# Kernel tuning notes

Hardware: AMD Instinct MI355X
Metric: run time of the kernel (lower is better)

Reference implementation:

```python
import jax, jax.numpy as jnp
import numpy as np

V, S, D, H = 32000, 1024, 768, 3072
EPS = 1e-5


def pos_encoding(seq_len, dim, dtype=jnp.float32):
    # pe[pos, i] = sin(pos/10000^(i/dim)) if i even else cos(pos/10000^(i/dim))
    pos = jnp.arange(seq_len, dtype=dtype)[:, None]
    i = jnp.arange(dim, dtype=dtype)[None, :]
    ang = pos / jnp.power(jnp.asarray(10000.0, dtype), i / dim)
    even = (jnp.arange(dim) % 2 == 0)[None, :]
    return jnp.where(even, jnp.sin(ang), jnp.cos(ang))


def layernorm2d(x, w, b):
    # normalizes over last two dims (token_size, input_dim), affine params [S, D]
    m = jnp.mean(x, axis=(-2, -1), keepdims=True)
    v = jnp.mean((x - m) ** 2, axis=(-2, -1), keepdims=True)
    return (x - m) / jnp.sqrt(v + EPS) * w + b


def setup_inputs() -> dict:
    key = jax.random.key(0)
    ks = jax.random.split(key, 16)
    sc = 0.02
    emb = jax.random.normal(ks[0], (V, D), jnp.float32) * sc
    emb = emb.at[0].set(0.0)  # padding_idx=0
    inp = {
        "x": jax.random.randint(ks[1], (8, S), 0, V),
        "emb": emb,
        "Wq": jax.random.normal(ks[2], (D, H), jnp.float32) * sc,
        "bq": jnp.zeros((H,), jnp.float32),
        "Wk": jax.random.normal(ks[3], (D, H), jnp.float32) * sc,
        "bk": jnp.zeros((H,), jnp.float32),
        "Wv": jax.random.normal(ks[4], (D, H), jnp.float32) * sc,
        "bv": jnp.zeros((H,), jnp.float32),
        "Wo": jax.random.normal(ks[5], (H, D), jnp.float32) * sc,
        "bo": jnp.zeros((D,), jnp.float32),
        "W1": jax.random.normal(ks[6], (D, H), jnp.float32) * sc,
        "b1": jnp.zeros((H,), jnp.float32),
        "W2": jax.random.normal(ks[7], (H, D), jnp.float32) * sc,
        "b2": jnp.zeros((D,), jnp.float32),
        "ln1_w": jnp.ones((S, D), jnp.float32),
        "ln1_b": jnp.zeros((S, D), jnp.float32),
        "ln2_w": jnp.ones((S, D), jnp.float32),
        "ln2_b": jnp.zeros((S, D), jnp.float32),
    }
    return inp


def reference(x, emb, Wq, bq, Wk, bk, Wv, bv, Wo, bo, W1, b1, W2, b2, ln1_w, ln1_b, ln2_w, ln2_b):
    y = emb[x]                                   # [B, S, D]
    y = y + pos_encoding(y.shape[1], y.shape[2], y.dtype)
    # unscaled self-attention (no 1/sqrt(d) factor, faithful to source)
    q = y @ Wq + bq
    k = y @ Wk + bk
    v = y @ Wv + bv
    attn = jax.nn.softmax(jnp.einsum("bsh,bth->bst", q, k), axis=-1)
    a = jnp.einsum("bst,bth->bsh", attn, v) @ Wo + bo
    y = layernorm2d(y + a, ln1_w, ln1_b)
    # FFN: GELU applied AFTER second linear (faithful to source)
    f = jax.nn.gelu((y @ W1 + b1) @ W2 + b2, approximate=False)
    y = layernorm2d(y + f, ln2_w, ln2_b)
    return y
```

## Files before the change

kernel.cpp:

```cpp
#include <hip/hip_runtime.h>
#include <hip/hip_fp16.h>

#define DI __device__ __forceinline__

typedef _Float16 f16x8 __attribute__((ext_vector_type(8)));
typedef float f32x4 __attribute__((ext_vector_type(4)));

struct alignas(8) h4 { __half x, y, z, w; };

DI void async16(const void* g, void* l) {
  __builtin_amdgcn_global_load_lds(
      (__attribute__((address_space(1))) void*)g,
      (__attribute__((address_space(3))) void*)l, 16, 0, 0);
}

DI float waveReduceSum(float v) {
#pragma unroll
  for (int i = 1; i < 64; i <<= 1) v += __shfl_xor(v, i);
  return v;
}
DI float waveReduceMax(float v) {
#pragma unroll
  for (int i = 1; i < 64; i <<= 1) v = fmaxf(v, __shfl_xor(v, i));
  return v;
}

DI float gelu_exact(float x) { return 0.5f * x * (1.f + erff(x * 0.70710678118654752f)); }

template <typename CT, bool BIAS, bool BROW>
__global__ __launch_bounds__(512, 2) void gemm_nt8(
    const __half* __restrict__ A, int lda, long long sA,
    const __half* __restrict__ Bt, int ldb, long long sB,
    const float* __restrict__ bias, long long sBias,
    CT* __restrict__ C, int ldc, long long sC,
    int nT, int K) {
  __shared__ __align__(16) __half As[2][16384];
  __shared__ __align__(16) __half Bs[2][16384];

  const int tid = threadIdx.x;
  const int wave = tid >> 6, lane = tid & 63;

  const int gsz = 4 * nT;
  const int g = blockIdx.x / gsz, r = blockIdx.x % gsz;
  const int m0 = (g * 4 + (r & 3)) * 256;
  const int n0 = (r >> 2) * 256;

  A += (long long)blockIdx.z * sA;
  Bt += (long long)blockIdx.z * sB;
  C += (long long)blockIdx.z * sC;
  if constexpr (BIAS || BROW) bias += (long long)blockIdx.z * sBias;

  const int wm = wave >> 2, wn = wave & 3;

  f32x4 acc[8][4];
#pragma unroll
  for (int i = 0; i < 8; ++i)
#pragma unroll
    for (int j = 0; j < 4; ++j) acc[i][j] = (f32x4){0.f, 0.f, 0.f, 0.f};

  const int srow = tid >> 3;
  const int gc = (tid & 7) ^ (srow & 7);
  const __half* Ag = A + (size_t)(m0 + srow) * lda + gc * 8;
  const __half* Bg = Bt + (size_t)(n0 + srow) * ldb + gc * 8;
  const size_t a64 = (size_t)64 * lda, b64 = (size_t)64 * ldb;
  char* AsW = (char*)As + wave * 1024;
  char* BsW = (char*)Bs + wave * 1024;

#define STG_A(t)                                                      \
  {                                                                   \
    const __half* s_ = Ag + (t) * 64;                                 \
    char* d_ = AsW + (((t) & 1) ? 32768 : 0);                         \
    async16(s_, d_);                                                  \
    async16(s_ + a64, d_ + 8192);                                     \
    async16(s_ + 2 * a64, d_ + 16384);                                \
    async16(s_ + 3 * a64, d_ + 24576);                                \
  }
#define STG_B(t)                                                      \
  {                                                                   \
    const __half* s_ = Bg + (t) * 64;                                 \
    char* d_ = BsW + (((t) & 1) ? 32768 : 0);                         \
    async16(s_, d_);                                                  \
    async16(s_ + b64, d_ + 8192);                                     \
    async16(s_ + 2 * b64, d_ + 16384);                                \
    async16(s_ + 3 * b64, d_ + 24576);                                \
  }

  const int ml = lane & 15, q = lane >> 4, lx = lane & 7;
  const int co0 = (q ^ lx) * 16, co1 = co0 ^ 64;
  const char* Ar = (const char*)As + wm * 16384 + ml * 128;
  const char* Br = (const char*)Bs + (wn >> 1) * 16384 + (wn & 1) * 8192 + ml * 128;

  const int nt = K >> 6;
  STG_A(0);
  STG_B(0);
  if (nt > 1) {
    STG_A(1);
    STG_B(1);
    asm volatile("s_waitcnt vmcnt(8)" ::: "memory");
  } else {
    asm volatile("s_waitcnt vmcnt(0)" ::: "memory");
  }
  __builtin_amdgcn_s_barrier();

  for (int t = 0; t < nt; ++t) {
    const int pb = (t & 1) ? 32768 : 0;
    const char* Ap = Ar + pb;
    const char* Bp = Br + pb;
    f16x8 a0[4], a1[4], a2[4], a3[4], b0[4], b1[4];

#pragma unroll
    for (int i = 0; i < 4; ++i) a0[i] = *(const f16x8*)(Ap + i * 2048 + co0);
#pragma unroll
    for (int j = 0; j < 4; ++j) b0[j] = *(const f16x8*)(Bp + j * 2048 + co0);
    __builtin_amdgcn_s_barrier();
    asm volatile("s_waitcnt lgkmcnt(0)" ::: "memory");
    __builtin_amdgcn_s_setprio(1);
#pragma unroll
    for (int i = 0; i < 4; ++i)
#pragma unroll
      for (int j = 0; j < 4; ++j)
        acc[i][j] = __builtin_amdgcn_mfma_f32_16x16x32_f16(a0[i], b0[j], acc[i][j], 0, 0, 0);
    __builtin_amdgcn_s_setprio(0);
    __builtin_amdgcn_s_barrier();

#pragma unroll
    for (int i = 0; i < 4; ++i) a1[i] = *(const f16x8*)(Ap + (4 + i) * 2048 + co0);
#pragma unroll
    for (int j = 0; j < 4; ++j) b1[j] = *(const f16x8*)(Bp + j * 2048 + co1);
    __builtin_amdgcn_s_barrier();
    asm volatile("s_waitcnt lgkmcnt(0)" ::: "memory");
    __builtin_amdgcn_s_setprio(1);
#pragma unroll
    for (int i = 0; i < 4; ++i)
#pragma unroll
      for (int j = 0; j < 4; ++j)
        acc[4 + i][j] = __builtin_amdgcn_mfma_f32_16x16x32_f16(a1[i], b0[j], acc[4 + i][j], 0, 0, 0);
    __builtin_amdgcn_s_setprio(0);
    __builtin_amdgcn_s_barrier();

#pragma unroll
    for (int i = 0; i < 4; ++i) a2[i] = *(const f16x8*)(Ap + i * 2048 + co1);
#pragma unroll
    for (int i = 0; i < 4; ++i) a3[i] = *(const f16x8*)(Ap + (4 + i) * 2048 + co1);
    if (t + 2 < nt) STG_B(t + 2);
    __builtin_amdgcn_s_barrier();
    asm volatile("s_waitcnt lgkmcnt(0)" ::: "memory");
    __builtin_amdgcn_s_setprio(1);
#pragma unroll
    for (int i = 0; i < 4; ++i)
#pragma unroll
      for (int j = 0; j < 4; ++j)
        acc[i][j] = __builtin_amdgcn_mfma_f32_16x16x32_f16(a2[i], b1[j], acc[i][j], 0, 0, 0);
    __builtin_amdgcn_s_setprio(0);
    __builtin_amdgcn_s_barrier();

    if (t + 2 < nt) {
      STG_A(t + 2);
      asm volatile("s_waitcnt vmcnt(8)" ::: "memory");
    } else if (t + 1 < nt) {
      asm volatile("s_waitcnt vmcnt(0)" ::: "memory");
    }
    __builtin_amdgcn_s_barrier();
    __builtin_amdgcn_s_setprio(1);
#pragma unroll
    for (int i = 0; i < 4; ++i)
#pragma unroll
      for (int j = 0; j < 4; ++j)
        acc[4 + i][j] = __builtin_amdgcn_mfma_f32_16x16x32_f16(a3[i], b1[j], acc[4 + i][j], 0, 0, 0);
    __builtin_amdgcn_s_setprio(0);
    __builtin_amdgcn_s_barrier();
  }
#undef STG_A
#undef STG_B

#pragma unroll
  for (int j = 0; j < 4; ++j) {
    const int col = n0 + wn * 64 + j * 16 + ml;
    const float bcol = BIAS ? bias[col] : 0.f;
#pragma unroll
    for (int i = 0; i < 8; ++i) {
      const int row = m0 + wm * 128 + i * 16 + q * 4;
#pragma unroll
      for (int rr = 0; rr < 4; ++rr) {
        float v = acc[i][j][rr] + bcol;
        if constexpr (BROW) v += bias[row + rr];
        if constexpr (sizeof(CT) == 4)
          C[(size_t)(row + rr) * ldc + col] = v;
        else
          C[(size_t)(row + rr) * ldc + col] = __float2half(v);
      }
    }
  }
}

template <typename CT, bool BIAS, bool BROW>
__global__ __launch_bounds__(256) void gemm_nt(
    const __half* __restrict__ A, int lda, long long sA,
    const __half* __restrict__ Bt, int ldb, long long sB,
    const float* __restrict__ bias, long long sBias,
    CT* __restrict__ C, int ldc, long long sC,
    int nT, int K) {
  __shared__ __align__(16) __half As[128 * 64];
  __shared__ __align__(16) __half Bs[128 * 64];

  const int tid = threadIdx.x;
  const int wave = tid >> 6, lane = tid & 63;

  const int gsz = 8 * nT;
  const int g = blockIdx.x / gsz, r = blockIdx.x % gsz;
  const int m0 = (g * 8 + (r & 7)) * 128;
  const int n0 = (r >> 3) * 128;

  A += (long long)blockIdx.z * sA;
  Bt += (long long)blockIdx.z * sB;
  C += (long long)blockIdx.z * sC;
  if constexpr (BIAS || BROW) bias += (long long)blockIdx.z * sBias;
  const int wm = wave & 1, wn = wave >> 1;

  f32x4 acc[4][4];
#pragma unroll
  for (int i = 0; i < 4; ++i)
#pragma unroll
    for (int jj = 0; jj < 4; ++jj) acc[i][jj] = (f32x4){0.f, 0.f, 0.f, 0.f};

  const int srow = tid >> 3;
  const int gc = (tid & 7) ^ (srow & 7);
  const __half* Ag = A + (size_t)(m0 + srow) * lda + gc * 8;
  const __half* Bg = Bt + (size_t)(n0 + srow) * ldb + gc * 8;
  const size_t a32 = (size_t)32 * lda, b32 = (size_t)32 * ldb;
  char* AsW = (char*)As + wave * 1024;
  char* BsW = (char*)Bs + wave * 1024;

  const int ml = lane & 15, q = lane >> 4, lx = lane & 7;
  const int aoff = ((wm * 64 + ml) * 8 + (q ^ lx)) * 16;
  const int boff = ((wn * 64 + ml) * 8 + (q ^ lx)) * 16;

  for (int k0 = 0; k0 < K; k0 += 64) {
#pragma unroll
    for (int i = 0; i < 4; ++i) {
      async16(Ag + i * a32 + k0, AsW + i * 4096);
      async16(Bg + i * b32 + k0, BsW + i * 4096);
    }
    __syncthreads();
#pragma unroll
    for (int jj = 0; jj < 2; ++jj) {
      const char* Ab = (const char*)As + (jj ? (aoff ^ 64) : aoff);
      const char* Bb = (const char*)Bs + (jj ? (boff ^ 64) : boff);
      f16x8 af[4], bf[4];
#pragma unroll
      for (int i = 0; i < 4; ++i) {
        af[i] = *(const f16x8*)(Ab + i * 2048);
        bf[i] = *(const f16x8*)(Bb + i * 2048);
      }
#pragma unroll
      for (int i = 0; i < 4; ++i)
#pragma unroll
        for (int jn = 0; jn < 4; ++jn)
          acc[i][jn] = __builtin_amdgcn_mfma_f32_16x16x32_f16(af[i], bf[jn], acc[i][jn], 0, 0, 0);
    }
    __syncthreads();
  }

#pragma unroll
  for (int jj = 0; jj < 4; ++jj) {
    const int col = n0 + wn * 64 + jj * 16 + ml;
    const float bcol = BIAS ? bias[col] : 0.f;
#pragma unroll
    for (int i = 0; i < 4; ++i) {
      const int row = m0 + wm * 64 + i * 16 + q * 4;
#pragma unroll
      for (int rr = 0; rr < 4; ++rr) {
        float v = acc[i][jj][rr] + bcol;
        if constexpr (BROW) v += bias[row + rr];
        if constexpr (sizeof(CT) == 4)
          C[(size_t)(row + rr) * ldc + col] = v;
        else
          C[(size_t)(row + rr) * ldc + col] = __float2half(v);
      }
    }
  }
}

__global__ __launch_bounds__(256) void prep(
    const float* __restrict__ Wq, const float* __restrict__ Wk,
    const float* __restrict__ Wv, const float* __restrict__ W1,
    const float* __restrict__ Wo, const float* __restrict__ W2,
    const float* __restrict__ bq, const float* __restrict__ bk,
    __half* __restrict__ wD, __half* __restrict__ wB, __half* __restrict__ wC,
    __half* __restrict__ wA, float* __restrict__ bqk) {
  if (blockIdx.x == 2304) {
    if (blockIdx.y == 0)
      for (int i = threadIdx.x; i < 3072; i += 256) {
        bqk[i] = bq[i];
        bqk[3072 + i] = bk[i];
      }
    return;
  }
  __shared__ float t[32][33];
  const int tx = threadIdx.x & 31, ty = threadIdx.x >> 5;
  if (blockIdx.y < 4) {
    const float* in;
    __half* out;
    switch (blockIdx.y) {
      case 0: in = Wq; out = wD; break;
      case 1: in = Wk; out = wD + 3072 * 768; break;
      case 2: in = Wv; out = wB; break;
      default: in = W1; out = wC; break;
    }
    const int cb = blockIdx.x % 96, rb = blockIdx.x / 96;
    const int c = cb * 32 + tx, r0 = rb * 32;
#pragma unroll
    for (int i = 0; i < 32; i += 8) t[ty + i][tx] = in[(size_t)(r0 + ty + i) * 3072 + c];
    __syncthreads();
    const int oc = r0 + tx, o0 = cb * 32;
#pragma unroll
    for (int i = 0; i < 32; i += 8)
      out[(size_t)(o0 + ty + i) * 768 + oc] = __float2half(t[tx][ty + i]);
  } else {
    const float* in = (blockIdx.y == 5) ? W2 : Wo;
    __half* out = wA + ((blockIdx.y == 5) ? 3072 * 768 : 0);
    const int cb = blockIdx.x % 24, rb = blockIdx.x / 24;
    const int c = cb * 32 + tx, r0 = rb * 32;
#pragma unroll
    for (int i = 0; i < 32; i += 8) t[ty + i][tx] = in[(size_t)(r0 + ty + i) * 768 + c];
    __syncthreads();
    const int oc = r0 + tx, o0 = cb * 32;
#pragma unroll
    for (int i = 0; i < 32; i += 8)
      out[(size_t)(o0 + ty + i) * 3072 + oc] = __float2half(t[tx][ty + i]);
  }
}

__global__ __launch_bounds__(256) void embed_pos_kernel(
    const int* __restrict__ x, const float* __restrict__ emb,
    float* __restrict__ y, __half* __restrict__ yh) {
  const int row = blockIdx.x;
  const int s = row & 1023;
  const int tok = x[row];
  const float* ep = emb + (size_t)tok * 768;
  float* yp = y + (size_t)row * 768;
  __half* hp = yh + (size_t)row * 768;
  const float c = -13.287712379549449f / 768.f;
  for (int d = threadIdx.x; d < 768; d += 256) {
    float ang = (float)s * exp2f((float)d * c);
    float pe = (d & 1) ? cosf(ang) : sinf(ang);
    float v = ep[d] + pe;
    yp[d] = v;
    hp[d] = __float2half(v);
  }
}

__global__ __launch_bounds__(256) void softmax_rows(
    const float* __restrict__ L, __half* __restrict__ P) {
  const size_t row = blockIdx.x;
  const float4 x = ((const float4*)(L + row * 1024))[threadIdx.x];
  const int wave = threadIdx.x >> 6, lane = threadIdx.x & 63;
  float m = fmaxf(fmaxf(x.x, x.y), fmaxf(x.z, x.w));
  m = waveReduceMax(m);
  __shared__ float sm[4];
  __shared__ float ssum[4];
  if (lane == 0) sm[wave] = m;
  __syncthreads();
  m = fmaxf(fmaxf(sm[0], sm[1]), fmaxf(sm[2], sm[3]));
  float e0 = expf(x.x - m), e1 = expf(x.y - m), e2 = expf(x.z - m), e3 = expf(x.w - m);
  float s = e0 + e1 + e2 + e3;
  s = waveReduceSum(s);
  if (lane == 0) ssum[wave] = s;
  __syncthreads();
  s = ssum[0] + ssum[1] + ssum[2] + ssum[3];
  const float inv = 1.f / s;
  h4 o{__float2half(e0 * inv), __float2half(e1 * inv), __float2half(e2 * inv),
       __float2half(e3 * inv)};
  ((h4*)(P + row * 1024))[threadIdx.x] = o;
}

template <bool GELU>
__global__ __launch_bounds__(256) void residual_stats(
    float* __restrict__ y, const float* __restrict__ p0, const float* __restrict__ p1,
    const float* __restrict__ bias, float2* __restrict__ partials) {
  const int b = blockIdx.y, chunk = blockIdx.x;
  const size_t base = (size_t)b * 786432 + (size_t)chunk * 8192;
  float4* yp = (float4*)(y + base);
  const float4* a0 = (const float4*)(p0 + base);
  const float4* a1 = (const float4*)(p1 + base);
  float s = 0.f, ss = 0.f;
#pragma unroll
  for (int it = 0; it < 8; ++it) {
    const int idx = it * 256 + threadIdx.x;
    const int d = (chunk * 8192 + it * 1024 + threadIdx.x * 4) % 768;
    float4 yv = yp[idx];
    float4 v0 = a0[idx];
    float4 v1 = a1[idx];
    const float4 bv = *(const float4*)(bias + d);
    float ax = v0.x + v1.x + bv.x, ay = v0.y + v1.y + bv.y;
    float az = v0.z + v1.z + bv.z, aw = v0.w + v1.w + bv.w;
    if constexpr (GELU) {
      ax = gelu_exact(ax); ay = gelu_exact(ay);
      az = gelu_exact(az); aw = gelu_exact(aw);
    }
    float4 r{yv.x + ax, yv.y + ay, yv.z + az, yv.w + aw};
    yp[idx] = r;
    s += r.x + r.y + r.z + r.w;
    ss += r.x * r.x + r.y * r.y + r.z * r.z + r.w * r.w;
  }
  s = waveReduceSum(s);
  ss = waveReduceSum(ss);
  __shared__ float2 wr[4];
  const int wave = threadIdx.x >> 6, lane = threadIdx.x & 63;
  if (lane == 0) wr[wave] = make_float2(s, ss);
  __syncthreads();
  if (threadIdx.x == 0) {
    float S = wr[0].x + wr[1].x + wr[2].x + wr[3].x;
    float SS = wr[0].y + wr[1].y + wr[2].y + wr[3].y;
    partials[b * 96 + chunk] = make_float2(S, SS);
  }
}

template <bool WB>
__global__ __launch_bounds__(256) void ln_apply(
    float* __restrict__ y, __half* __restrict__ yh, const float* __restrict__ w,
    const float* __restrict__ bb, const float2* __restrict__ partials) {
  const unsigned i4 = blockIdx.x * 256 + threadIdx.x;
  const unsigned i = i4 * 4;
  const unsigned b = i / 786432u;
  const int tid = threadIdx.x;
  float s = 0.f, ss = 0.f;
  if (tid < 96) {
    float2 p = partials[b * 96 + tid];
    s = p.x;
    ss = p.y;
  }
  s = waveReduceSum(s);
  ss = waveReduceSum(ss);
  __shared__ float2 wsum[4];
  if ((tid & 63) == 0) wsum[tid >> 6] = make_float2(s, ss);
  __syncthreads();
  const float S = wsum[0].x + wsum[1].x + wsum[2].x + wsum[3].x;
  const float SS = wsum[0].y + wsum[1].y + wsum[2].y + wsum[3].y;
  const float inv = 1.f / 786432.f;
  const float mean = S * inv;
  const float rstd = rsqrtf(SS * inv - mean * mean + 1e-5f);

  const unsigned e4 = (i - b * 786432u) >> 2;
  float4 yv = ((const float4*)y)[i4];
  const float4 wv = ((const float4*)w)[e4];
  const float4 bv = ((const float4*)bb)[e4];
  float4 r;
  r.x = (yv.x - mean) * rstd * wv.x + bv.x;
  r.y = (yv.y - mean) * rstd * wv.y + bv.y;
  r.z = (yv.z - mean) * rstd * wv.z + bv.z;
  r.w = (yv.w - mean) * rstd * wv.w + bv.w;
  ((float4*)y)[i4] = r;
  if constexpr (WB) {
    h4 o{__float2half(r.x), __float2half(r.y), __float2half(r.z), __float2half(r.w)};
    ((h4*)yh)[i4] = o;
  }
}

extern "C" void kernel_launch(void* const* d_in, const int* in_sizes, int n_in,
                              void* d_out, int out_size, void* d_ws, size_t ws_size,
                              hipStream_t stream) {
  const int* x = (const int*)d_in[0];
  const float* emb = (const float*)d_in[1];
  const float* Wq = (const float*)d_in[2];
  const float* bq = (const float*)d_in[3];
  const float* Wk = (const float*)d_in[4];
  const float* bk = (const float*)d_in[5];
  const float* Wv = (const float*)d_in[6];
  const float* bv = (const float*)d_in[7];
  const float* Wo = (const float*)d_in[8];
  const float* bo = (const float*)d_in[9];
  const float* W1 = (const float*)d_in[10];
  const float* b1 = (const float*)d_in[11];
  const float* W2 = (const float*)d_in[12];
  const float* b2 = (const float*)d_in[13];
  const float* ln1w = (const float*)d_in[14];
  const float* ln1b = (const float*)d_in[15];
  const float* ln2w = (const float*)d_in[16];
  const float* ln2b = (const float*)d_in[17];

  float* y = (float*)d_out;

  char* ws = (char*)d_ws;
  __half* yh = (__half*)(ws + 0);
  __half* qb = (__half*)(ws + 12582912);
  __half* kb = (__half*)(ws + 62914560);
  __half* Ph = kb;
  __half* vT = (__half*)(ws + 113246208);
  float* abuf = (float*)vT;
  float* Lg = (float*)(ws + 163577856);
  __half* wA = (__half*)(ws + 197132288);
  __half* wD = (__half*)(ws + 206569472);
  __half* wB = (__half*)(ws + 216006656);
  __half* wC = (__half*)(ws + 220725248);
  float* bqk = (float*)(ws + 225443840);
  float2* part = (float2*)(ws + 225468416);
  const size_t WS_NEEDED = 225474624;
  if (ws_size < WS_NEEDED) return;

  const dim3 blk(256), blk8(512);
  const long long SH = 1024LL * 3072, SS = 1024LL * 1024;
  const long long HALF = 25165824;
  float* p1 = abuf + 6291456;

  prep<<<dim3(2305, 6), blk, 0, stream>>>(Wq, Wk, Wv, W1, Wo, W2, bq, bk, wD, wB, wC, wA, bqk);
  embed_pos_kernel<<<dim3(8192), blk, 0, stream>>>(x, emb, y, yh);

  gemm_nt8<__half, true, false><<<dim3(384, 1, 2), blk8, 0, stream>>>(
      yh, 768, 0, wD, 768, 3072LL * 768, bqk, 3072, qb, 3072, HALF, 12, 768);

  gemm_nt8<__half, false, true><<<dim3(48, 1, 8), blk8, 0, stream>>>(
      wB, 768, 0, yh, 768, 1024LL * 768, bv, 0, vT, 1024, SH, 4, 768);

  gemm_nt<float, false, false><<<dim3(64, 1, 8), blk, 0, stream>>>(
      qb, 3072, SH, kb, 3072, SH, nullptr, 0, Lg, 1024, SS, 8, 3072);

  softmax_rows<<<dim3(8192), blk, 0, stream>>>(Lg, Ph);

  gemm_nt8<__half, false, false><<<dim3(48, 1, 8), blk8, 0, stream>>>(
      Ph, 1024, SS, vT, 1024, SH, nullptr, 0, (__half*)qb, 3072, SH, 12, 1024);

  gemm_nt8<float, false, false><<<dim3(96, 1, 2), blk8, 0, stream>>>(
      (__half*)qb, 3072, 1536, wA, 3072, 1536, nullptr, 0, abuf, 768, 6291456, 3, 1536);

  residual_stats<false><<<dim3(96, 8), blk, 0, stream>>>(y, abuf, p1, bo, part);
  ln_apply<true><<<dim3(6144), blk, 0, stream>>>(y, yh, ln1w, ln1b, part);

  gemm_nt8<__half, true, false><<<dim3(384, 1, 1), blk8, 0, stream>>>(
      yh, 768, 0, wC, 768, 0, b1, 0, (__half*)qb, 3072, 0, 12, 768);
  gemm_nt8<float, false, false><<<dim3(96, 1, 2), blk8, 0, stream>>>(
      (__half*)qb, 3072, 1536, wA + 3072 * 768, 3072, 1536, nullptr, 0, abuf, 768, 6291456, 3, 1536);

  residual_stats<true><<<dim3(96, 8), blk, 0, stream>>>(y, abuf, p1, b2, part);
  ln_apply<false><<<dim3(6144), blk, 0, stream>>>(y, nullptr, ln2w, ln2b, part);
}
```

Measured before the change: 836.2 us.

## Software-pipeline LDS fragment reads in gemm_nt8 and use smaller-tile GEMMs for narrow shapes

The 8-wave GEMM main loop is restructured into a two-stage register double buffer. The next half-K fragments are read from LDS while MFMAs run on the current ones, which cuts the per-iteration barriers from eight to two and issues both global tile loads together. Separately, the V projection, P·V and both output-projection GEMMs switch from the large-tile 512-thread kernel to the 256-thread gemm_nt kernel with more blocks, so that under-filled launches occupy more CUs. The double buffer roughly doubles fragment register use, which risks lower occupancy or spills.

```diff
diff --git a/kernel.cpp b/kernel.cpp
--- a/kernel.cpp
+++ b/kernel.cpp
@@ -90,6 +90,29 @@
   const char* Ar = (const char*)As + wm * 16384 + ml * 128;
   const char* Br = (const char*)Bs + (wn >> 1) * 16384 + (wn & 1) * 8192 + ml * 128;
 
+#define RDFRAGS(av_, bv_, pb_, co_)                                   \
+  {                                                                   \
+    const char* Ap_ = Ar + (pb_);                                     \
+    const char* Bp_ = Br + (pb_);                                     \
+    _Pragma("unroll") for (int i_ = 0; i_ < 8; ++i_)                  \
+        av_[i_] = *(const f16x8*)(Ap_ + i_ * 2048 + (co_));           \
+    _Pragma("unroll") for (int j_ = 0; j_ < 4; ++j_)                  \
+        bv_[j_] = *(const f16x8*)(Bp_ + j_ * 2048 + (co_));           \
+  }
+
+#define DOMFMA(av_, bv_)                                              \
+  {                                                                   \
+    __builtin_amdgcn_s_setprio(1);                                    \
+    _Pragma("unroll") for (int i_ = 0; i_ < 8; ++i_)                  \
+        _Pragma("unroll") for (int j_ = 0; j_ < 4; ++j_)              \
+            acc[i_][j_] = __builtin_amdgcn_mfma_f32_16x16x32_f16(     \
+                av_[i_], bv_[j_], acc[i_][j_], 0, 0, 0);              \
+    __builtin_amdgcn_s_setprio(0);                                    \
+  }
+
+  f16x8 aX[8], bX[4];
+  f16x8 aY[8], bY[4];
+
   const int nt = K >> 6;
   STG_A(0);
   STG_B(0);
@@ -101,77 +124,31 @@
     asm volatile("s_waitcnt vmcnt(0)" ::: "memory");
   }
   __builtin_amdgcn_s_barrier();
+  RDFRAGS(aX, bX, 0, co0);
 
   for (int t = 0; t < nt; ++t) {
     const int pb = (t & 1) ? 32768 : 0;
-    const char* Ap = Ar + pb;
-    const char* Bp = Br + pb;
-    f16x8 a0[4], a1[4], a2[4], a3[4], b0[4], b1[4];
-
-#pragma unroll
-    for (int i = 0; i < 4; ++i) a0[i] = *(const f16x8*)(Ap + i * 2048 + co0);
-#pragma unroll
-    for (int j = 0; j < 4; ++j) b0[j] = *(const f16x8*)(Bp + j * 2048 + co0);
+    const int pn = pb ^ 32768;
+    RDFRAGS(aY, bY, pb, co1);
+    DOMFMA(aX, bX);
+    asm volatile("s_waitcnt lgkmcnt(0)" ::: "memory");
+    __builtin_amdgcn_sched_barrier(0);
     __builtin_amdgcn_s_barrier();
-    asm volatile("s_waitcnt lgkmcnt(0)" ::: "memory");
-    __builtin_amdgcn_s_setprio(1);
-#pragma unroll
-    for (int i = 0; i < 4; ++i)
-#pragma unroll
-      for (int j = 0; j < 4; ++j)
-        acc[i][j] = __builtin_amdgcn_mfma_f32_16x16x32_f16(a0[i], b0[j], acc[i][j], 0, 0, 0);
-    __builtin_amdgcn_s_setprio(0);
-    __builtin_amdgcn_s_barrier();
-
-#pragma unroll
-    for (int i = 0; i < 4; ++i) a1[i] = *(const f16x8*)(Ap + (4 + i) * 2048 + co0);
-#pragma unroll
-    for (int j = 0; j < 4; ++j) b1[j] = *(const f16x8*)(Bp + j * 2048 + co1);
-    __builtin_amdgcn_s_barrier();
-    asm volatile("s_waitcnt lgkmcnt(0)" ::: "memory");
-    __builtin_amdgcn_s_setprio(1);
-#pragma unroll
-    for (int i = 0; i < 4; ++i)
-#pragma unroll
-      for (int j = 0; j < 4; ++j)
-        acc[4 + i][j] = __builtin_amdgcn_mfma_f32_16x16x32_f16(a1[i], b0[j], acc[4 + i][j], 0, 0, 0);
-    __builtin_amdgcn_s_setprio(0);
-    __builtin_amdgcn_s_barrier();
-
-#pragma unroll
-    for (int i = 0; i < 4; ++i) a2[i] = *(const f16x8*)(Ap + i * 2048 + co1);
-#pragma unroll
-    for (int i = 0; i < 4; ++i) a3[i] = *(const f16x8*)(Ap + (4 + i) * 2048 + co1);
-    if (t + 2 < nt) STG_B(t + 2);
-    __builtin_amdgcn_s_barrier();
-    asm volatile("s_waitcnt lgkmcnt(0)" ::: "memory");
-    __builtin_amdgcn_s_setprio(1);
-#pragma unroll
-    for (int i = 0; i < 4; ++i)
-#pragma unroll
-      for (int j = 0; j < 4; ++j)
-        acc[i][j] = __builtin_amdgcn_mfma_f32_16x16x32_f16(a2[i], b1[j], acc[i][j], 0, 0, 0);
-    __builtin_amdgcn_s_setprio(0);
-    __builtin_amdgcn_s_barrier();
-
     if (t + 2 < nt) {
       STG_A(t + 2);
+      STG_B(t + 2);
       asm volatile("s_waitcnt vmcnt(8)" ::: "memory");
     } else if (t + 1 < nt) {
       asm volatile("s_waitcnt vmcnt(0)" ::: "memory");
     }
     __builtin_amdgcn_s_barrier();
-    __builtin_amdgcn_s_setprio(1);
-#pragma unroll
-    for (int i = 0; i < 4; ++i)
-#pragma unroll
-      for (int j = 0; j < 4; ++j)
-        acc[4 + i][j] = __builtin_amdgcn_mfma_f32_16x16x32_f16(a3[i], b1[j], acc[4 + i][j], 0, 0, 0);
-    __builtin_amdgcn_s_setprio(0);
-    __builtin_amdgcn_s_barrier();
+    if (t + 1 < nt) RDFRAGS(aX, bX, pn, co0);
+    DOMFMA(aY, bY);
   }
 #undef STG_A
 #undef STG_B
+#undef RDFRAGS
+#undef DOMFMA
 
 #pragma unroll
   for (int j = 0; j < 4; ++j) {
@@ -509,27 +486,27 @@
   gemm_nt8<__half, true, false><<<dim3(384, 1, 2), blk8, 0, stream>>>(
       yh, 768, 0, wD, 768, 3072LL * 768, bqk, 3072, qb, 3072, HALF, 12, 768);
 
-  gemm_nt8<__half, false, true><<<dim3(48, 1, 8), blk8, 0, stream>>>(
-      wB, 768, 0, yh, 768, 1024LL * 768, bv, 0, vT, 1024, SH, 4, 768);
+  gemm_nt<__half, false, true><<<dim3(192, 1, 8), blk, 0, stream>>>(
+      wB, 768, 0, yh, 768, 1024LL * 768, bv, 0, vT, 1024, SH, 8, 768);
 
   gemm_nt<float, false, false><<<dim3(64, 1, 8), blk, 0, stream>>>(
       qb, 3072, SH, kb, 3072, SH, nullptr, 0, Lg, 1024, SS, 8, 3072);
 
   softmax_rows<<<dim3(8192), blk, 0, stream>>>(Lg, Ph);
 
-  gemm_nt8<__half, false, false><<<dim3(48, 1, 8), blk8, 0, stream>>>(
-      Ph, 1024, SS, vT, 1024, SH, nullptr, 0, (__half*)qb, 3072, SH, 12, 1024);
-
-  gemm_nt8<float, false, false><<<dim3(96, 1, 2), blk8, 0, stream>>>(
-      (__half*)qb, 3072, 1536, wA, 3072, 1536, nullptr, 0, abuf, 768, 6291456, 3, 1536);
+  gemm_nt<__half, false, false><<<dim3(192, 1, 8), blk, 0, stream>>>(
+      Ph, 1024, SS, vT, 1024, SH, nullptr, 0, (__half*)qb, 3072, SH, 24, 1024);
+
+  gemm_nt<float, false, false><<<dim3(384, 1, 2), blk, 0, stream>>>(
+      (__half*)qb, 3072, 1536, wA, 3072, 1536, nullptr, 0, abuf, 768, 6291456, 6, 1536);
 
   residual_stats<false><<<dim3(96, 8), blk, 0, stream>>>(y, abuf, p1, bo, part);
   ln_apply<true><<<dim3(6144), blk, 0, stream>>>(y, yh, ln1w, ln1b, part);
 
   gemm_nt8<__half, true, false><<<dim3(384, 1, 1), blk8, 0, stream>>>(
       yh, 768, 0, wC, 768, 0, b1, 0, (__half*)qb, 3072, 0, 12, 768);
-  gemm_nt8<float, false, false><<<dim3(96, 1, 2), blk8, 0, stream>>>(
-      (__half*)qb, 3072, 1536, wA + 3072 * 768, 3072, 1536, nullptr, 0, abuf, 768, 6291456, 3, 1536);
+  gemm_nt<float, false, false><<<dim3(384, 1, 2), blk, 0, stream>>>(
+      (__half*)qb, 3072, 1536, wA + 3072 * 768, 3072, 1536, nullptr, 0, abuf, 768, 6291456, 6, 1536);
 
   residual_stats<true><<<dim3(96, 8), blk, 0, stream>>>(y, abuf, p1, b2, part);
   ln_apply<false><<<dim3(6144), blk, 0, stream>>>(y, nullptr, ln2w, ln2b, part);
```

Result: faster. 756.6 us (-9.5%).
